# Optimization experiments

Measured on AMD Instinct MI355X. Metric: run time of the kernel, lower is better.

## Reference

```python
import jax, jax.numpy as jnp
import numpy as np

B, S, D = 2, 1024, 1024
E = 8          # routed experts
I = 1024       # per-expert intermediate
IS = 1024      # shared expert intermediate
TOP_K = 2
NUM_SHARED = 1


def setup_inputs() -> dict:
    key = jax.random.key(0)
    ks = jax.random.split(key, 8)
    scale = 0.02
    return {
        "x": jax.random.normal(ks[0], (B, S, D), dtype=jnp.float32),
        "w_gate": jax.random.normal(ks[1], (D, E), dtype=jnp.float32) * scale,
        "wg": jax.random.normal(ks[2], (E, D, I), dtype=jnp.float32) * scale,  # expert gate_proj
        "wu": jax.random.normal(ks[3], (E, D, I), dtype=jnp.float32) * scale,  # expert up_proj
        "wd": jax.random.normal(ks[4], (E, I, D), dtype=jnp.float32) * scale,  # expert down_proj
        "ws_g": jax.random.normal(ks[5], (NUM_SHARED, D, IS), dtype=jnp.float32) * scale,
        "ws_u": jax.random.normal(ks[6], (NUM_SHARED, D, IS), dtype=jnp.float32) * scale,
        "ws_d": jax.random.normal(ks[7], (NUM_SHARED, IS, D), dtype=jnp.float32) * scale,
    }


def _swiglu(t, w_gate_proj, w_up, w_down):
    # t: [N, D]
    g = t @ w_gate_proj            # [N, I]
    u = t @ w_up                   # [N, I]
    return (jax.nn.silu(g) * u) @ w_down  # [N, D]


def reference(x, w_gate, wg, wu, wd, ws_g, ws_u, ws_d):
    Bb, Ss, Dd = x.shape
    x_flat = x.reshape(Bb * Ss, Dd)                  # [N, D]
    N = x_flat.shape[0]

    # --- router ---
    logits = x_flat @ w_gate                          # [N, E]
    topk_logits, topk_idx = jax.lax.top_k(logits, TOP_K)
    topk_w = jax.nn.softmax(topk_logits, axis=-1)     # [N, K]

    # --- aux load-balancing loss ---
    one_hot = jax.nn.one_hot(topk_idx, E, dtype=jnp.float32)  # [N, K, E]
    f = one_hot.sum(axis=1).mean(axis=0)                       # [E]
    P = jax.nn.softmax(logits, axis=-1).mean(axis=0)           # [E]
    aux_loss = E * jnp.sum(f * P)

    # --- combine weights: cw[n, e] = sum_k topk_w[n,k] * 1[topk_idx[n,k]==e] ---
    cw = jnp.einsum("nk,nke->ne", topk_w, one_hot)             # [N, E]

    # --- routed experts: dense compute over all experts, weighted combine ---
    g = jnp.einsum("nd,edi->eni", x_flat, wg)                  # [E, N, I]
    u = jnp.einsum("nd,edi->eni", x_flat, wu)                  # [E, N, I]
    a = jax.nn.silu(g) * u                                     # [E, N, I]
    y = jnp.einsum("eni,eid->end", a, wd)                      # [E, N, D]
    routed = jnp.einsum("ne,end->nd", cw, y)                   # [N, D]

    # --- shared experts ---
    shared = jnp.zeros_like(x_flat)
    for s in range(NUM_SHARED):
        shared = shared + _swiglu(x_flat, ws_g[s], ws_u[s], ws_d[s])

    out = (routed + shared).reshape(Bb, Ss, Dd)
    return out, aux_loss
```

## Files before the change

kernel.cpp:

```cpp
#include <hip/hip_runtime.h>
#include <math.h>

typedef unsigned short u16;
typedef __attribute__((ext_vector_type(8))) short short8;
typedef __attribute__((ext_vector_type(4))) float f32x4;
typedef __attribute__((ext_vector_type(4))) unsigned short u16x4;
typedef __attribute__((ext_vector_type(8))) unsigned short u16x8;

#define N_TOK 2048
#define DIM 1024
#define OUT_ELEMS 2097152

#define GLDS16(gp, lp) __builtin_amdgcn_global_load_lds( \
    (const __attribute__((address_space(1))) unsigned int*)(gp), \
    (__attribute__((address_space(3))) unsigned int*)(lp), 16, 0, 0)

__device__ __forceinline__ u16 f2bf(float f) {
    union { float f; unsigned u; } v; v.f = f;
    unsigned r = (v.u + 0x7FFFu + ((v.u >> 16) & 1u)) >> 16;
    return (u16)r;
}
__device__ __forceinline__ float bf2f(u16 h) {
    union { unsigned u; float f; } v; v.u = ((unsigned)h) << 16;
    return v.f;
}

__global__ void k_init(int* __restrict__ tlist, int* __restrict__ curs,
                       float* __restrict__ Psum, int* __restrict__ cnt8) {
    int i = blockIdx.x * 256 + threadIdx.x;
    tlist[4096 + i] = i;
    if (i < 16) curs[i] = 0;
    if (i < 8) { Psum[i] = 0.f; cnt8[i] = 0; }
}

__global__ void k_cvt_w(const float* __restrict__ wg, const float* __restrict__ wu,
                        const float* __restrict__ wd, const float* __restrict__ wsg,
                        const float* __restrict__ wsu, const float* __restrict__ wsd,
                        u16* __restrict__ wgt, u16* __restrict__ wut,
                        u16* __restrict__ wdt, u16* __restrict__ wsgt,
                        u16* __restrict__ wsut, u16* __restrict__ wsdt) {
    __shared__ u16 tile[8 * 1024];
    int bx = blockIdx.x;
    int mat = bx >> 7;
    int chunk = bx & 127;
    const float* src; u16* dst;
    if      (mat <  8) { src = wg  + (size_t)mat * 1048576;        dst = wgt + (size_t)mat * 1048576; }
    else if (mat < 16) { src = wu  + (size_t)(mat - 8) * 1048576;  dst = wut + (size_t)(mat - 8) * 1048576; }
    else if (mat < 24) { src = wd  + (size_t)(mat - 16) * 1048576; dst = wdt + (size_t)(mat - 16) * 1048576; }
    else if (mat == 24){ src = wsg; dst = wsgt; }
    else if (mat == 25){ src = wsu; dst = wsut; }
    else               { src = wsd; dst = wsdt; }
    const float* srow = src + (size_t)chunk * 8192;
    u16* dchunk = dst + (size_t)chunk * 8192;
    int t = threadIdx.x;
    int r  = t >> 5;
    int c0 = (t & 31) * 4;
    f32x4 v[8];
#pragma unroll
    for (int j = 0; j < 8; j++)
        v[j] = *(const f32x4*)(srow + r * 1024 + c0 + j * 128);
#pragma unroll
    for (int j = 0; j < 8; j++) {
        u16x4 o;
        o.x = f2bf(v[j].x); o.y = f2bf(v[j].y); o.z = f2bf(v[j].z); o.w = f2bf(v[j].w);
        *(u16x4*)(tile + r * 1024 + c0 + j * 128) = o;
    }
    __syncthreads();
#pragma unroll
    for (int j = 0; j < 4; j++) {
        int n = t + j * 256;
        u16x8 o;
#pragma unroll
        for (int k = 0; k < 8; k++) o[k] = tile[k * 1024 + n];
        *(u16x8*)(dchunk + n * 8) = o;
    }
}

__global__ void k_router(const float* __restrict__ x, const float* __restrict__ wgate,
                         u16* __restrict__ xb, int* __restrict__ tidx,
                         float* __restrict__ tw, float* __restrict__ Psum,
                         int* __restrict__ cnt8) {
    __shared__ float sP[8];
    __shared__ int   sC[8];
    int t = threadIdx.x;
    if (t < 8) { sP[t] = 0.f; sC[t] = 0; }
    __syncthreads();
    int wave = t >> 6;
    int lane = t & 63;
    int n = blockIdx.x * 4 + wave;
    const float* xr = x + (size_t)n * DIM;
    u16* xbr = xb + (size_t)n * DIM;
    float acc[8] = {0.f,0.f,0.f,0.f,0.f,0.f,0.f,0.f};
#pragma unroll
    for (int i = 0; i < 16; i++) {
        int d = lane + i * 64;
        float xv = xr[d];
        xbr[d] = f2bf(xv);
        const float* wr = wgate + d * 8;
#pragma unroll
        for (int e = 0; e < 8; e++) acc[e] += xv * wr[e];
    }
#pragma unroll
    for (int off = 32; off; off >>= 1) {
#pragma unroll
        for (int e = 0; e < 8; e++) acc[e] += __shfl_xor(acc[e], off);
    }
    if (lane == 0) {
        float mx = acc[0];
#pragma unroll
        for (int e = 1; e < 8; e++) mx = fmaxf(mx, acc[e]);
        float p[8], s = 0.f;
#pragma unroll
        for (int e = 0; e < 8; e++) { p[e] = expf(acc[e] - mx); s += p[e]; }
        float inv = 1.f / s;
#pragma unroll
        for (int e = 0; e < 8; e++) atomicAdd(&sP[e], p[e] * inv);
        int i0 = 0; float b0 = acc[0];
#pragma unroll
        for (int e = 1; e < 8; e++) if (acc[e] > b0) { b0 = acc[e]; i0 = e; }
        int i1 = -1; float b1 = -3.4e38f;
#pragma unroll
        for (int e = 0; e < 8; e++) if (e != i0 && acc[e] > b1) { b1 = acc[e]; i1 = e; }
        float w0 = 1.f / (1.f + expf(b1 - b0));
        tidx[n * 2] = i0; tidx[n * 2 + 1] = i1;
        tw[n * 2] = w0;   tw[n * 2 + 1] = 1.f - w0;
        atomicAdd(&sC[i0], 1);
        atomicAdd(&sC[i1], 1);
    }
    __syncthreads();
    if (t < 8) {
        atomicAdd(&Psum[t], sP[t]);
        atomicAdd(&cnt8[t], sC[t]);
    }
}

__global__ void k_scatter(const int* __restrict__ tidx, const float* __restrict__ Psum,
                          const int* __restrict__ cnt8, int* __restrict__ curs,
                          int* __restrict__ tlist, int* __restrict__ slots,
                          float* __restrict__ out, int* __restrict__ counts,
                          int* __restrict__ offs) {
    __shared__ int s_off[8];
    int t = threadIdx.x;
    if (t == 0) {
        int o = 0;
        for (int e = 0; e < 8; e++) { s_off[e] = o; o += cnt8[e]; }
    }
    __syncthreads();
    if (blockIdx.x == 0 && t == 0) {
        float aux = 0.f;
        for (int e = 0; e < 8; e++) {
            int c = cnt8[e];
            aux += (float)c * Psum[e];
            offs[e] = s_off[e]; counts[e] = c;
        }
        out[OUT_ELEMS] = 8.f * aux / ((float)N_TOK * (float)N_TOK);
        offs[8] = 4096; counts[8] = 2048;
    }
    int n = blockIdx.x * 256 + t;
    if (n < N_TOK) {
#pragma unroll
        for (int k = 0; k < 2; k++) {
            int e = tidx[n * 2 + k];
            int p = atomicAdd(&curs[e], 1);
            int sl = s_off[e] + p;
            tlist[sl] = n;
            slots[n * 2 + k] = sl;
        }
    }
}

__global__ __launch_bounds__(256, 2)
void k_gemm1(const u16* __restrict__ xb, const u16* __restrict__ wgt,
             const u16* __restrict__ wut, const u16* __restrict__ wsgt,
             const u16* __restrict__ wsut, const int* __restrict__ tlist,
             const int* __restrict__ counts, const int* __restrict__ offs,
             u16* __restrict__ H) {
    int bx = blockIdx.x;
    int job = bx >> 7;
    int mt = (bx >> 3) & 15;
    int nt = bx & 7;
    int jcnt = counts[job];
    int m0 = mt << 7;
    if (m0 >= jcnt) return;
    int joff = offs[job];
    int n0 = nt << 7;
    const u16* Bg = (job < 8) ? (wgt + (size_t)job * 1048576) : wsgt;
    const u16* Bu = (job < 8) ? (wut + (size_t)job * 1048576) : wsut;

    __shared__ __attribute__((aligned(128))) u16 As[4096];
    __shared__ __attribute__((aligned(128))) u16 Bgs[4096];
    __shared__ __attribute__((aligned(128))) u16 Bus[4096];

    int t = threadIdx.x;
    int wave = t >> 6, lane = t & 63;
    int ch = (lane & 3) * 8;
    int r0 = (wave * 2 + 0) * 16 + (lane >> 2);
    int r1 = (wave * 2 + 1) * 16 + (lane >> 2);
    int tok0 = tlist[joff + m0 + r0];
    int tok1 = tlist[joff + m0 + r1];
    const u16* a0 = xb + (size_t)tok0 * 1024 + ch;
    const u16* a1 = xb + (size_t)tok1 * 1024 + ch;
    const u16* gB = Bg + (size_t)wave * 8192 + (size_t)(n0 + lane) * 8;
    const u16* uB = Bu + (size_t)wave * 8192 + (size_t)(n0 + lane) * 8;
    u16* lA0 = As  + (wave * 2 + 0) * 512;  u16* lA1 = As  + (wave * 2 + 1) * 512;
    u16* lGa = Bgs + wave * 1024;           u16* lGb = Bgs + wave * 1024 + 512;
    u16* lUa = Bus + wave * 1024;           u16* lUb = Bus + wave * 1024 + 512;

    int wm = (wave >> 1) << 6, wn = (wave & 1) << 6;
    int quad = lane >> 4, lr = lane & 15;

    f32x4 accg[4][4], accu[4][4];
    f32x4 zz = {0.f, 0.f, 0.f, 0.f};
#pragma unroll
    for (int i = 0; i < 4; i++)
#pragma unroll
        for (int j = 0; j < 4; j++) { accg[i][j] = zz; accu[i][j] = zz; }

    for (int k0 = 0; k0 < 1024; k0 += 32) {
        size_t koff = (size_t)k0 * 1024;
        GLDS16(a0 + k0, lA0);        GLDS16(a1 + k0, lA1);
        GLDS16(gB + koff, lGa);      GLDS16(gB + koff + 512, lGb);
        GLDS16(uB + koff, lUa);      GLDS16(uB + koff + 512, lUb);
        __syncthreads();
        short8 af[4], bgf[4], buf[4];
#pragma unroll
        for (int i = 0; i < 4; i++) {
            int nrow = wn + i * 16 + lr;
            af[i]  = *(const short8*)(As  + (wm + i * 16 + lr) * 32 + quad * 8);
            bgf[i] = *(const short8*)(Bgs + quad * 1024 + nrow * 8);
            buf[i] = *(const short8*)(Bus + quad * 1024 + nrow * 8);
        }
#pragma unroll
        for (int mi = 0; mi < 4; mi++)
#pragma unroll
            for (int ni = 0; ni < 4; ni++) {
                accg[mi][ni] = __builtin_amdgcn_mfma_f32_16x16x32_bf16(af[mi], bgf[ni], accg[mi][ni], 0, 0, 0);
                accu[mi][ni] = __builtin_amdgcn_mfma_f32_16x16x32_bf16(af[mi], buf[ni], accu[mi][ni], 0, 0, 0);
            }
        __syncthreads();
    }
#pragma unroll
    for (int mi = 0; mi < 4; mi++) {
        int rowb = m0 + wm + mi * 16 + quad * 4;
#pragma unroll
        for (int rr = 0; rr < 4; rr++) {
            int row = rowb + rr;
            if (row < jcnt) {
                size_t base = (size_t)(joff + row) * 1024 + n0 + wn;
#pragma unroll
                for (int ni = 0; ni < 4; ni++) {
                    float g = accg[mi][ni][rr];
                    float u = accu[mi][ni][rr];
                    float h = (g / (1.f + expf(-g))) * u;
                    H[base + ni * 16 + lr] = f2bf(h);
                }
            }
        }
    }
}

__global__ __launch_bounds__(256, 2)
void k_gemm2(const u16* __restrict__ H, const u16* __restrict__ wdt,
             const u16* __restrict__ wsdt, const int* __restrict__ counts,
             const int* __restrict__ offs, u16* __restrict__ Y) {
    int bx = blockIdx.x;
    int job = bx >> 7;
    int mt = (bx >> 3) & 15;
    int nt = bx & 7;
    int jcnt = counts[job];
    int m0 = mt << 7;
    if (m0 >= jcnt) return;
    int joff = offs[job];
    int n0 = nt << 7;
    const u16* Bt = (job < 8) ? (wdt + (size_t)job * 1048576) : wsdt;

    __shared__ __attribute__((aligned(128))) u16 As[4096];
    __shared__ __attribute__((aligned(128))) u16 Bs[4096];

    int t = threadIdx.x;
    int wave = t >> 6, lane = t & 63;
    int ch = (lane & 3) * 8;
    int r0 = (wave * 2 + 0) * 16 + (lane >> 2);
    int r1 = (wave * 2 + 1) * 16 + (lane >> 2);
    const u16* a0 = H + (size_t)(joff + m0 + r0) * 1024 + ch;
    const u16* a1 = H + (size_t)(joff + m0 + r1) * 1024 + ch;
    const u16* bB = Bt + (size_t)wave * 8192 + (size_t)(n0 + lane) * 8;
    u16* lA0 = As + (wave * 2 + 0) * 512;  u16* lA1 = As + (wave * 2 + 1) * 512;
    u16* lBa = Bs + wave * 1024;           u16* lBb = Bs + wave * 1024 + 512;

    int wm = (wave >> 1) << 6, wn = (wave & 1) << 6;
    int quad = lane >> 4, lr = lane & 15;

    f32x4 acc[4][4];
    f32x4 zz = {0.f, 0.f, 0.f, 0.f};
#pragma unroll
    for (int i = 0; i < 4; i++)
#pragma unroll
        for (int j = 0; j < 4; j++) acc[i][j] = zz;

    for (int k0 = 0; k0 < 1024; k0 += 32) {
        size_t koff = (size_t)k0 * 1024;
        GLDS16(a0 + k0, lA0);    GLDS16(a1 + k0, lA1);
        GLDS16(bB + koff, lBa);  GLDS16(bB + koff + 512, lBb);
        __syncthreads();
        short8 af[4], bf[4];
#pragma unroll
        for (int i = 0; i < 4; i++) {
            af[i] = *(const short8*)(As + (wm + i * 16 + lr) * 32 + quad * 8);
            bf[i] = *(const short8*)(Bs + quad * 1024 + (wn + i * 16 + lr) * 8);
        }
#pragma unroll
        for (int mi = 0; mi < 4; mi++)
#pragma unroll
            for (int ni = 0; ni < 4; ni++)
                acc[mi][ni] = __builtin_amdgcn_mfma_f32_16x16x32_bf16(af[mi], bf[ni], acc[mi][ni], 0, 0, 0);
        __syncthreads();
    }
#pragma unroll
    for (int mi = 0; mi < 4; mi++) {
        int rowb = m0 + wm + mi * 16 + quad * 4;
#pragma unroll
        for (int rr = 0; rr < 4; rr++) {
            int row = rowb + rr;
            if (row < jcnt) {
                u16* yrow = Y + (size_t)(joff + row) * 1024 + n0 + wn;
#pragma unroll
                for (int ni = 0; ni < 4; ni++)
                    yrow[ni * 16 + lr] = f2bf(acc[mi][ni][rr]);
            }
        }
    }
}

__global__ void k_combine(const u16* __restrict__ Y, const int* __restrict__ slots,
                          const float* __restrict__ tw, float* __restrict__ out) {
    int n = blockIdx.x;
    int d = threadIdx.x;
    int s0 = slots[n * 2], s1 = slots[n * 2 + 1];
    float w0 = tw[n * 2], w1 = tw[n * 2 + 1];
    u16x4 y0 = ((const u16x4*)(Y + (size_t)s0 * 1024))[d];
    u16x4 y1 = ((const u16x4*)(Y + (size_t)s1 * 1024))[d];
    u16x4 ys = ((const u16x4*)(Y + (size_t)(4096 + n) * 1024))[d];
    f32x4 r;
    r.x = w0 * bf2f(y0.x) + w1 * bf2f(y1.x) + bf2f(ys.x);
    r.y = w0 * bf2f(y0.y) + w1 * bf2f(y1.y) + bf2f(ys.y);
    r.z = w0 * bf2f(y0.z) + w1 * bf2f(y1.z) + bf2f(ys.z);
    r.w = w0 * bf2f(y0.w) + w1 * bf2f(y1.w) + bf2f(ys.w);
    ((f32x4*)(out + (size_t)n * 1024))[d] = r;
}

extern "C" void kernel_launch(void* const* d_in, const int* in_sizes, int n_in,
                              void* d_out, int out_size, void* d_ws, size_t ws_size,
                              hipStream_t stream) {
    const float* x     = (const float*)d_in[0];
    const float* wgate = (const float*)d_in[1];
    const float* wg    = (const float*)d_in[2];
    const float* wu    = (const float*)d_in[3];
    const float* wd    = (const float*)d_in[4];
    const float* wsg   = (const float*)d_in[5];
    const float* wsu   = (const float*)d_in[6];
    const float* wsd   = (const float*)d_in[7];
    float* out = (float*)d_out;

    char* ws = (char*)d_ws;
    u16*   xb    = (u16*)(ws + 0);
    u16*   wgt   = (u16*)(ws + 4194304);
    u16*   wut   = (u16*)(ws + 20971520);
    u16*   wdt   = (u16*)(ws + 37748736);
    u16*   wsgt  = (u16*)(ws + 54525952);
    u16*   wsut  = (u16*)(ws + 56623104);
    u16*   wsdt  = (u16*)(ws + 58720256);
    u16*   H     = (u16*)(ws + 60817408);
    u16*   Y     = (u16*)(ws + 4194304);
    int*   tidx  = (int*)(ws + 73400320);
    float* tw    = (float*)(ws + 73416704);
    int*   tlist = (int*)(ws + 73433088);
    int*   slots = (int*)(ws + 73457664);
    int*   counts= (int*)(ws + 73474048);
    int*   offs  = (int*)(ws + 73474112);
    int*   curs  = (int*)(ws + 73474176);
    float* Psum  = (float*)(ws + 73474240);
    int*   cnt8  = (int*)(ws + 73474304);

    k_init<<<8, 256, 0, stream>>>(tlist, curs, Psum, cnt8);
    k_router<<<512, 256, 0, stream>>>(x, wgate, xb, tidx, tw, Psum, cnt8);
    k_scatter<<<8, 256, 0, stream>>>(tidx, Psum, cnt8, curs, tlist, slots,
                                     out, counts, offs);
    k_cvt_w<<<3456, 256, 0, stream>>>(wg, wu, wd, wsg, wsu, wsd,
                                      wgt, wut, wdt, wsgt, wsut, wsdt);
    k_gemm1<<<1152, 256, 0, stream>>>(xb, wgt, wut, wsgt, wsut, tlist, counts, offs, H);
    k_gemm2<<<1152, 256, 0, stream>>>(H, wdt, wsdt, counts, offs, Y);
    k_combine<<<2048, 256, 0, stream>>>(Y, slots, tw, out);
}
```

Before: 267.9 us.

## Fuse router, init and weight conversion; overlap down-proj conversion with gemm1

```diff
diff --git a/kernel.cpp b/kernel.cpp
--- a/kernel.cpp
+++ b/kernel.cpp
@@ -25,69 +25,64 @@
     return v.f;
 }
 
-__global__ void k_init(int* __restrict__ tlist, int* __restrict__ curs,
-                       float* __restrict__ Psum, int* __restrict__ cnt8) {
-    int i = blockIdx.x * 256 + threadIdx.x;
-    tlist[4096 + i] = i;
-    if (i < 16) curs[i] = 0;
-    if (i < 8) { Psum[i] = 0.f; cnt8[i] = 0; }
-}
-
-__global__ void k_cvt_w(const float* __restrict__ wg, const float* __restrict__ wu,
-                        const float* __restrict__ wd, const float* __restrict__ wsg,
-                        const float* __restrict__ wsu, const float* __restrict__ wsd,
-                        u16* __restrict__ wgt, u16* __restrict__ wut,
-                        u16* __restrict__ wdt, u16* __restrict__ wsgt,
-                        u16* __restrict__ wsut, u16* __restrict__ wsdt) {
-    __shared__ u16 tile[8 * 1024];
+__device__ __forceinline__ void cvt_chunk(const float* __restrict__ src,
+                                          u16* __restrict__ dst, int chunk,
+                                          char* smem, int t) {
+    float* tile = (float*)smem;
+    const char* gsrc = (const char*)(src + (size_t)chunk * 8192);
+    u16* dchunk = dst + (size_t)chunk * 8192;
+    int w = t >> 6, l = t & 63;
+#pragma unroll
+    for (int j = 0; j < 8; j++) {
+        int idx = w * 8 + j;
+        GLDS16(gsrc + idx * 1024 + l * 16, smem + idx * 1024);
+    }
+    __syncthreads();
+    int n0 = (t & 63) * 4 + (t >> 6) * 256;
+    f32x4 v[8];
+#pragma unroll
+    for (int k = 0; k < 8; k++)
+        v[k] = *(const f32x4*)(tile + k * 1024 + n0);
+#pragma unroll
+    for (int i = 0; i < 4; i++) {
+        u16x8 o;
+#pragma unroll
+        for (int k = 0; k < 8; k++) o[k] = f2bf(v[k][i]);
+        *(u16x8*)(dchunk + (size_t)(n0 + i) * 8) = o;
+    }
+}
+
+__global__ __launch_bounds__(256)
+void k_front(const float* __restrict__ wg, const float* __restrict__ wu,
+             const float* __restrict__ wsg, const float* __restrict__ wsu,
+             u16* __restrict__ wgt, u16* __restrict__ wut,
+             u16* __restrict__ wsgt, u16* __restrict__ wsut,
+             const float* __restrict__ x, const float* __restrict__ wgate,
+             u16* __restrict__ xb, int* __restrict__ tidx, float* __restrict__ tw,
+             float* __restrict__ Pp, int* __restrict__ Cp,
+             int* __restrict__ tlist, int* __restrict__ curs) {
+    __shared__ __attribute__((aligned(128))) char smem[32768];
     int bx = blockIdx.x;
-    int mat = bx >> 7;
-    int chunk = bx & 127;
-    const float* src; u16* dst;
-    if      (mat <  8) { src = wg  + (size_t)mat * 1048576;        dst = wgt + (size_t)mat * 1048576; }
-    else if (mat < 16) { src = wu  + (size_t)(mat - 8) * 1048576;  dst = wut + (size_t)(mat - 8) * 1048576; }
-    else if (mat < 24) { src = wd  + (size_t)(mat - 16) * 1048576; dst = wdt + (size_t)(mat - 16) * 1048576; }
-    else if (mat == 24){ src = wsg; dst = wsgt; }
-    else if (mat == 25){ src = wsu; dst = wsut; }
-    else               { src = wsd; dst = wsdt; }
-    const float* srow = src + (size_t)chunk * 8192;
-    u16* dchunk = dst + (size_t)chunk * 8192;
     int t = threadIdx.x;
-    int r  = t >> 5;
-    int c0 = (t & 31) * 4;
-    f32x4 v[8];
-#pragma unroll
-    for (int j = 0; j < 8; j++)
-        v[j] = *(const f32x4*)(srow + r * 1024 + c0 + j * 128);
-#pragma unroll
-    for (int j = 0; j < 8; j++) {
-        u16x4 o;
-        o.x = f2bf(v[j].x); o.y = f2bf(v[j].y); o.z = f2bf(v[j].z); o.w = f2bf(v[j].w);
-        *(u16x4*)(tile + r * 1024 + c0 + j * 128) = o;
-    }
-    __syncthreads();
-#pragma unroll
-    for (int j = 0; j < 4; j++) {
-        int n = t + j * 256;
-        u16x8 o;
-#pragma unroll
-        for (int k = 0; k < 8; k++) o[k] = tile[k * 1024 + n];
-        *(u16x8*)(dchunk + n * 8) = o;
-    }
-}
-
-__global__ void k_router(const float* __restrict__ x, const float* __restrict__ wgate,
-                         u16* __restrict__ xb, int* __restrict__ tidx,
-                         float* __restrict__ tw, float* __restrict__ Psum,
-                         int* __restrict__ cnt8) {
-    __shared__ float sP[8];
-    __shared__ int   sC[8];
-    int t = threadIdx.x;
+    if (bx < 2304) {
+        int mat = bx >> 7, chunk = bx & 127;
+        const float* src; u16* dst;
+        if      (mat <  8) { src = wg + (size_t)mat * 1048576;       dst = wgt + (size_t)mat * 1048576; }
+        else if (mat < 16) { src = wu + (size_t)(mat - 8) * 1048576; dst = wut + (size_t)(mat - 8) * 1048576; }
+        else if (mat == 16){ src = wsg; dst = wsgt; }
+        else               { src = wsu; dst = wsut; }
+        cvt_chunk(src, dst, chunk, smem, t);
+        return;
+    }
+    int b = bx - 2304;
+    float* sP = (float*)smem;
+    int*   sC = (int*)(smem + 64);
     if (t < 8) { sP[t] = 0.f; sC[t] = 0; }
+    if (b == 0 && t < 16) curs[t] = 0;
     __syncthreads();
     int wave = t >> 6;
     int lane = t & 63;
-    int n = blockIdx.x * 4 + wave;
+    int n = b * 4 + wave;
     const float* xr = x + (size_t)n * DIM;
     u16* xbr = xb + (size_t)n * DIM;
     float acc[8] = {0.f,0.f,0.f,0.f,0.f,0.f,0.f,0.f};
@@ -106,6 +101,7 @@
         for (int e = 0; e < 8; e++) acc[e] += __shfl_xor(acc[e], off);
     }
     if (lane == 0) {
+        tlist[4096 + n] = n;
         float mx = acc[0];
 #pragma unroll
         for (int e = 1; e < 8; e++) mx = fmaxf(mx, acc[e]);
@@ -128,30 +124,46 @@
         atomicAdd(&sC[i1], 1);
     }
     __syncthreads();
-    if (t < 8) {
-        atomicAdd(&Psum[t], sP[t]);
-        atomicAdd(&cnt8[t], sC[t]);
-    }
-}
-
-__global__ void k_scatter(const int* __restrict__ tidx, const float* __restrict__ Psum,
-                          const int* __restrict__ cnt8, int* __restrict__ curs,
+    if (t < 8) { Pp[b * 8 + t] = sP[t]; Cp[b * 8 + t] = sC[t]; }
+}
+
+__global__ void k_scatter(const int* __restrict__ tidx, const float* __restrict__ Pp,
+                          const int* __restrict__ Cp, int* __restrict__ curs,
                           int* __restrict__ tlist, int* __restrict__ slots,
                           float* __restrict__ out, int* __restrict__ counts,
                           int* __restrict__ offs) {
-    __shared__ int s_off[8];
+    __shared__ int   s_off[8];
+    __shared__ int   sCnt[8];
+    __shared__ float sPs[8];
+    __shared__ int   redC[256];
+    __shared__ float redP[256];
     int t = threadIdx.x;
+    int e = t & 7, g = t >> 3;
+    int cs = 0; float ps = 0.f;
+#pragma unroll
+    for (int j = 0; j < 16; j++) {
+        int b = g + j * 32;
+        cs += Cp[b * 8 + e];
+        ps += Pp[b * 8 + e];
+    }
+    redC[t] = cs; redP[t] = ps;
+    __syncthreads();
+    if (t < 8) {
+        int c = 0; float p = 0.f;
+        for (int g2 = 0; g2 < 32; g2++) { c += redC[g2 * 8 + t]; p += redP[g2 * 8 + t]; }
+        sCnt[t] = c; sPs[t] = p;
+    }
+    __syncthreads();
     if (t == 0) {
         int o = 0;
-        for (int e = 0; e < 8; e++) { s_off[e] = o; o += cnt8[e]; }
+        for (int e2 = 0; e2 < 8; e2++) { s_off[e2] = o; o += sCnt[e2]; }
     }
     __syncthreads();
     if (blockIdx.x == 0 && t == 0) {
         float aux = 0.f;
-        for (int e = 0; e < 8; e++) {
-            int c = cnt8[e];
-            aux += (float)c * Psum[e];
-            offs[e] = s_off[e]; counts[e] = c;
+        for (int e2 = 0; e2 < 8; e2++) {
+            aux += (float)sCnt[e2] * sPs[e2];
+            offs[e2] = s_off[e2]; counts[e2] = sCnt[e2];
         }
         out[OUT_ELEMS] = 8.f * aux / ((float)N_TOK * (float)N_TOK);
         offs[8] = 4096; counts[8] = 2048;
@@ -160,9 +172,9 @@
     if (n < N_TOK) {
 #pragma unroll
         for (int k = 0; k < 2; k++) {
-            int e = tidx[n * 2 + k];
-            int p = atomicAdd(&curs[e], 1);
-            int sl = s_off[e] + p;
+            int ee = tidx[n * 2 + k];
+            int p = atomicAdd(&curs[ee], 1);
+            int sl = s_off[ee] + p;
             tlist[sl] = n;
             slots[n * 2 + k] = sl;
         }
@@ -174,11 +186,23 @@
              const u16* __restrict__ wut, const u16* __restrict__ wsgt,
              const u16* __restrict__ wsut, const int* __restrict__ tlist,
              const int* __restrict__ counts, const int* __restrict__ offs,
-             u16* __restrict__ H) {
+             u16* __restrict__ H,
+             const float* __restrict__ wd, const float* __restrict__ wsd,
+             u16* __restrict__ wdt, u16* __restrict__ wsdt) {
+    __shared__ __attribute__((aligned(128))) char smem[32768];
     int bx = blockIdx.x;
-    int job = bx >> 7;
-    int mt = (bx >> 3) & 15;
-    int nt = bx & 7;
+    int t = threadIdx.x;
+    if (bx < 1152) {
+        int mat = bx >> 7, chunk = bx & 127;
+        const float* src = (mat < 8) ? (wd + (size_t)mat * 1048576) : wsd;
+        u16* dst = (mat < 8) ? (wdt + (size_t)mat * 1048576) : wsdt;
+        cvt_chunk(src, dst, chunk, smem, t);
+        return;
+    }
+    int bg = bx - 1152;
+    int job = bg >> 7;
+    int mt = (bg >> 3) & 15;
+    int nt = bg & 7;
     int jcnt = counts[job];
     int m0 = mt << 7;
     if (m0 >= jcnt) return;
@@ -187,11 +211,10 @@
     const u16* Bg = (job < 8) ? (wgt + (size_t)job * 1048576) : wsgt;
     const u16* Bu = (job < 8) ? (wut + (size_t)job * 1048576) : wsut;
 
-    __shared__ __attribute__((aligned(128))) u16 As[4096];
-    __shared__ __attribute__((aligned(128))) u16 Bgs[4096];
-    __shared__ __attribute__((aligned(128))) u16 Bus[4096];
-
-    int t = threadIdx.x;
+    u16* As  = (u16*)smem;
+    u16* Bgs = (u16*)(smem + 8192);
+    u16* Bus = (u16*)(smem + 16384);
+
     int wave = t >> 6, lane = t & 63;
     int ch = (lane & 3) * 8;
     int r0 = (wave * 2 + 0) * 16 + (lane >> 2);
@@ -379,16 +402,15 @@
     int*   counts= (int*)(ws + 73474048);
     int*   offs  = (int*)(ws + 73474112);
     int*   curs  = (int*)(ws + 73474176);
-    float* Psum  = (float*)(ws + 73474240);
-    int*   cnt8  = (int*)(ws + 73474304);
-
-    k_init<<<8, 256, 0, stream>>>(tlist, curs, Psum, cnt8);
-    k_router<<<512, 256, 0, stream>>>(x, wgate, xb, tidx, tw, Psum, cnt8);
-    k_scatter<<<8, 256, 0, stream>>>(tidx, Psum, cnt8, curs, tlist, slots,
+    float* Pp    = (float*)(ws + 73474304);
+    int*   Cp    = (int*)(ws + 73490688);
+
+    k_front<<<2816, 256, 0, stream>>>(wg, wu, wsg, wsu, wgt, wut, wsgt, wsut,
+                                      x, wgate, xb, tidx, tw, Pp, Cp, tlist, curs);
+    k_scatter<<<8, 256, 0, stream>>>(tidx, Pp, Cp, curs, tlist, slots,
                                      out, counts, offs);
-    k_cvt_w<<<3456, 256, 0, stream>>>(wg, wu, wd, wsg, wsu, wsd,
-                                      wgt, wut, wdt, wsgt, wsut, wsdt);
-    k_gemm1<<<1152, 256, 0, stream>>>(xb, wgt, wut, wsgt, wsut, tlist, counts, offs, H);
+    k_gemm1<<<2304, 256, 0, stream>>>(xb, wgt, wut, wsgt, wsut, tlist, counts, offs,
+                                      H, wd, wsd, wdt, wsdt);
     k_gemm2<<<1152, 256, 0, stream>>>(H, wdt, wsdt, counts, offs, Y);
     k_combine<<<2048, 256, 0, stream>>>(Y, slots, tw, out);
 }
```

Result: no change. 264.4 us (-1.3%).
